# Optimization experiments

Measured on AMD Instinct MI355X. Metric: run time of the kernel, lower is better.

Reference implementation:

```python
import jax, jax.numpy as jnp
import numpy as np

EPS = 1e-06

def phi(x):
    # canonical linear-attention feature map: elu(x) + 1 (positive features)
    return jax.nn.elu(x) + 1.0

def setup_inputs() -> dict:
    key = jax.random.key(0)
    kq, kk, kv = jax.random.split(key, 3)
    B, H, S, D = 4, 16, 4096, 64
    query = jax.random.normal(kq, (B, H, S, D), dtype=jnp.float32)
    k = jax.random.normal(kk, (B, H, S, D), dtype=jnp.float32)
    value = jax.random.normal(kv, (B, H, S, D), dtype=jnp.float32)
    attention_mask = jnp.ones((B, S), dtype=jnp.float32)
    return {"query": query, "key": k, "value": value, "attention_mask": attention_mask}

def reference(query, key, value, attention_mask):
    B, H, S, D = query.shape
    q = query / jnp.sqrt(jnp.asarray(D, query.dtype))
    phi_q = phi(q)                                   # [b,h,n,d]
    phi_k = phi(key)                                 # [b,h,n,d]
    mask = attention_mask[:, None, :, None].astype(phi_k.dtype)  # [b,1,n,1]
    phi_k = phi_k * mask
    kv_term = jnp.einsum('bhnd,bhnv->bhdv', phi_k, value)        # [b,h,d,v]
    output = jnp.einsum('bhnd,bhdv->bhnv', phi_q, kv_term)       # [b,h,n,v]
    k_one = jnp.sum(phi_k, axis=2)                               # [b,h,d] == phi_k @ masked ones
    normalizer = jnp.einsum('bhnd,bhd->bhn', phi_q, k_one)[..., None]  # [b,h,n,1]
    return output / (normalizer + EPS)
```

## Files before the change

### kernel.cpp

```cpp
#include <hip/hip_runtime.h>

typedef unsigned short ushort_t;
typedef unsigned int uint32;
typedef __bf16 bf16x8 __attribute__((ext_vector_type(8)));
typedef float f32x4 __attribute__((ext_vector_type(4)));

#define NB 4
#define NH 16
#define NS 4096
#define ND 64
#define NBH 64
#define EPSF 1e-6f

#define CH1 16
#define ROWS1 (NS / CH1)
#define P2R 128
#define LDJ 70
#define LDJW 35

__device__ __forceinline__ float phi_f(float x) {
    return x > 0.0f ? x + 1.0f : __expf(x);
}
__device__ __forceinline__ ushort_t bf16_rn(float x) {
    uint32 u = __float_as_uint(x);
    uint32 r = (u + 0x7FFFu + ((u >> 16) & 1u)) >> 16;
    return (ushort_t)r;
}
__device__ __forceinline__ void split2(float x, ushort_t& h, ushort_t& l) {
    h = bf16_rn(x);
    float hf = __uint_as_float(((uint32)h) << 16);
    l = bf16_rn(x - hf);
}
union FragU { uint32 u[4]; bf16x8 v; };
__device__ __forceinline__ bf16x8 ld_frag(const ushort_t* arr, int widx) {
    const uint32* p = (const uint32*)arr;
    FragU f;
    f.u[0] = p[widx]; f.u[1] = p[widx + 1]; f.u[2] = p[widx + 2]; f.u[3] = p[widx + 3];
    return f.v;
}
__device__ __forceinline__ f32x4 mfma16(bf16x8 a, bf16x8 b, f32x4 c) {
    return __builtin_amdgcn_mfma_f32_16x16x32_bf16(a, b, c, 0, 0, 0);
}

template<bool PART>
__global__ __launch_bounds__(256)
void la_pass1(const float* __restrict__ Kin, const float* __restrict__ Vin,
              const float* __restrict__ Min, float* __restrict__ okv,
              float* __restrict__ ok1)
{
    const int t  = threadIdx.x;
    const int cx = blockIdx.x;
    const int bh = blockIdx.y;
    const int bb = bh >> 4;
    const float* Kb = Kin + (long long)bh * NS * ND;
    const float* Vb = Vin + (long long)bh * NS * ND;
    const float* Mb = Min + (long long)bb * NS;

    __shared__ __align__(16) ushort_t skh[64 * LDJ], skl[64 * LDJ];
    __shared__ __align__(16) ushort_t svh[64 * LDJ], svl[64 * LDJ];

    const int p  = t & 31;
    const int c0 = (t >> 5) * 8;
    const int wv = t >> 6;
    const int m  = t & 15;
    const int q  = (t & 63) >> 4;
    const int lane = t & 63;

    const f32x4 zf = {0.f, 0.f, 0.f, 0.f};
    f32x4 acc0 = zf, acc1 = zf, acc2 = zf, acc3 = zf;
    float k1loc[8] = {0.f,0.f,0.f,0.f,0.f,0.f,0.f,0.f};

    const int s0 = cx * ROWS1;

    for (int tile = 0; tile < ROWS1 / 64; ++tile) {
        const int rb = s0 + tile * 64;
        __syncthreads();
        {
            const int r0 = rb + 2 * p;
            const float4 ka = *(const float4*)(Kb + (long long)r0 * ND + c0);
            const float4 kb2 = *(const float4*)(Kb + (long long)r0 * ND + c0 + 4);
            const float4 kc = *(const float4*)(Kb + (long long)(r0 + 1) * ND + c0);
            const float4 kd = *(const float4*)(Kb + (long long)(r0 + 1) * ND + c0 + 4);
            const float4 va = *(const float4*)(Vb + (long long)r0 * ND + c0);
            const float4 vb2 = *(const float4*)(Vb + (long long)r0 * ND + c0 + 4);
            const float4 vc = *(const float4*)(Vb + (long long)(r0 + 1) * ND + c0);
            const float4 vd = *(const float4*)(Vb + (long long)(r0 + 1) * ND + c0 + 4);
            const float m0 = Mb[r0], m1 = Mb[r0 + 1];
            const float kr0[8] = {ka.x,ka.y,ka.z,ka.w,kb2.x,kb2.y,kb2.z,kb2.w};
            const float kr1[8] = {kc.x,kc.y,kc.z,kc.w,kd.x,kd.y,kd.z,kd.w};
            const float vr0[8] = {va.x,va.y,va.z,va.w,vb2.x,vb2.y,vb2.z,vb2.w};
            const float vr1[8] = {vc.x,vc.y,vc.z,vc.w,vd.x,vd.y,vd.z,vd.w};
            #pragma unroll
            for (int i = 0; i < 8; ++i) {
                const float x0 = phi_f(kr0[i]) * m0;
                const float x1 = phi_f(kr1[i]) * m1;
                k1loc[i] += x0 + x1;
                ushort_t h0, l0, h1, l1;
                split2(x0, h0, l0); split2(x1, h1, l1);
                const int widx = (c0 + i) * LDJW + p;
                ((uint32*)skh)[widx] = (uint32)h0 | ((uint32)h1 << 16);
                ((uint32*)skl)[widx] = (uint32)l0 | ((uint32)l1 << 16);
                split2(vr0[i], h0, l0); split2(vr1[i], h1, l1);
                ((uint32*)svh)[widx] = (uint32)h0 | ((uint32)h1 << 16);
                ((uint32*)svl)[widx] = (uint32)l0 | ((uint32)l1 << 16);
            }
        }
        __syncthreads();
        #pragma unroll
        for (int ks = 0; ks < 2; ++ks) {
            const int fo = ks * 16 + q * 4;
            const bf16x8 ah = ld_frag(skh, (16 * wv + m) * LDJW + fo);
            const bf16x8 al = ld_frag(skl, (16 * wv + m) * LDJW + fo);
            {
                const bf16x8 fbh = ld_frag(svh, (0 + m) * LDJW + fo);
                const bf16x8 fbl = ld_frag(svl, (0 + m) * LDJW + fo);
                acc0 = mfma16(al, fbh, acc0); acc0 = mfma16(ah, fbl, acc0); acc0 = mfma16(ah, fbh, acc0);
            }
            {
                const bf16x8 fbh = ld_frag(svh, (16 + m) * LDJW + fo);
                const bf16x8 fbl = ld_frag(svl, (16 + m) * LDJW + fo);
                acc1 = mfma16(al, fbh, acc1); acc1 = mfma16(ah, fbl, acc1); acc1 = mfma16(ah, fbh, acc1);
            }
            {
                const bf16x8 fbh = ld_frag(svh, (32 + m) * LDJW + fo);
                const bf16x8 fbl = ld_frag(svl, (32 + m) * LDJW + fo);
                acc2 = mfma16(al, fbh, acc2); acc2 = mfma16(ah, fbl, acc2); acc2 = mfma16(ah, fbh, acc2);
            }
            {
                const bf16x8 fbh = ld_frag(svh, (48 + m) * LDJW + fo);
                const bf16x8 fbl = ld_frag(svl, (48 + m) * LDJW + fo);
                acc3 = mfma16(al, fbh, acc3); acc3 = mfma16(ah, fbl, acc3); acc3 = mfma16(ah, fbh, acc3);
            }
        }
    }

    const int dbase = 16 * wv + q * 4;
    if (PART) {
        float* outp = okv + (long long)(bh * CH1 + cx) * (ND * ND);
        #pragma unroll
        for (int i = 0; i < 4; ++i) {
            outp[(dbase + i) * ND +  0 + m] = acc0[i];
            outp[(dbase + i) * ND + 16 + m] = acc1[i];
            outp[(dbase + i) * ND + 32 + m] = acc2[i];
            outp[(dbase + i) * ND + 48 + m] = acc3[i];
        }
    } else {
        float* outp = okv + (long long)bh * (ND * ND);
        #pragma unroll
        for (int i = 0; i < 4; ++i) {
            atomicAdd(&outp[(dbase + i) * ND +  0 + m], acc0[i]);
            atomicAdd(&outp[(dbase + i) * ND + 16 + m], acc1[i]);
            atomicAdd(&outp[(dbase + i) * ND + 32 + m], acc2[i]);
            atomicAdd(&outp[(dbase + i) * ND + 48 + m], acc3[i]);
        }
    }
    __syncthreads();
    float* red = (float*)skh;
    #pragma unroll
    for (int i = 0; i < 8; ++i) red[(c0 + i) * 33 + p] = k1loc[i];
    __syncthreads();
    if (t < 64) {
        float s = 0.f;
        #pragma unroll
        for (int pp = 0; pp < 32; ++pp) s += red[t * 33 + pp];
        if (PART) ok1[(bh * CH1 + cx) * ND + t] = s;
        else      atomicAdd(&ok1[bh * ND + t], s);
    }
}

__global__ __launch_bounds__(256)
void la_reduce(const float* __restrict__ pkv, const float* __restrict__ pk1,
               float* __restrict__ kv, float* __restrict__ k1)
{
    const int t = threadIdx.x;
    const int bh = blockIdx.x;
    const float4* src = (const float4*)(pkv + (long long)bh * CH1 * ND * ND);
    float4 a[4];
    #pragma unroll
    for (int i = 0; i < 4; ++i) { a[i].x = 0.f; a[i].y = 0.f; a[i].z = 0.f; a[i].w = 0.f; }
    for (int c = 0; c < CH1; ++c) {
        #pragma unroll
        for (int i = 0; i < 4; ++i) {
            const float4 v = src[c * 1024 + t + 256 * i];
            a[i].x += v.x; a[i].y += v.y; a[i].z += v.z; a[i].w += v.w;
        }
    }
    float4* dst = (float4*)(kv + (long long)bh * ND * ND);
    #pragma unroll
    for (int i = 0; i < 4; ++i) dst[t + 256 * i] = a[i];
    if (t < ND) {
        float s = 0.f;
        for (int c = 0; c < CH1; ++c) s += pk1[(bh * CH1 + c) * ND + t];
        k1[bh * ND + t] = s;
    }
}

__global__ __launch_bounds__(256)
void la_pass2(const float* __restrict__ Qin, const float* __restrict__ KVin,
              const float* __restrict__ K1in, float* __restrict__ Out)
{
    const int t  = threadIdx.x;
    const int bh = blockIdx.y;
    const int s0 = blockIdx.x * P2R;
    const long long base = (long long)bh * NS * ND;

    __shared__ __align__(16) ushort_t sAh[P2R * LDJ], sAl[P2R * LDJ];
    __shared__ __align__(16) ushort_t sBh[80 * LDJ],  sBl[80 * LDJ];

    {
        const float* KVb = KVin + (long long)bh * ND * ND;
        const int d  = t >> 4;
        const int v4 = (t & 15) * 4;
        #pragma unroll
        for (int it = 0; it < 4; ++it) {
            const int dd = d + 16 * it;
            const float4 kv = *(const float4*)(KVb + dd * ND + v4);
            const float vals[4] = {kv.x, kv.y, kv.z, kv.w};
            #pragma unroll
            for (int i = 0; i < 4; ++i) {
                ushort_t h, l; split2(vals[i], h, l);
                sBh[(v4 + i) * LDJ + dd] = h;
                sBl[(v4 + i) * LDJ + dd] = l;
            }
        }
        if (t < 64) {
            ushort_t h, l; split2(K1in[bh * ND + t], h, l);
            sBh[64 * LDJ + t] = h; sBl[64 * LDJ + t] = l;
        }
        for (int z = t; z < 15 * 64; z += 256) {
            const int n  = 65 + (z >> 6);
            const int dd = z & 63;
            sBh[n * LDJ + dd] = 0; sBl[n * LDJ + dd] = 0;
        }
    }
    {
        const int lr = t >> 4;
        const int lc = (t & 15) * 4;
        #pragma unroll
        for (int it = 0; it < 8; ++it) {
            const int r = lr + 16 * it;
            const float4 q4 = *(const float4*)(Qin + base + (long long)(s0 + r) * ND + lc);
            const float xs[4] = {q4.x, q4.y, q4.z, q4.w};
            ushort_t h[4], l[4];
            #pragma unroll
            for (int i = 0; i < 4; ++i) split2(phi_f(xs[i] * 0.125f), h[i], l[i]);
            const int w0 = (r * LDJ + lc) >> 1;
            ((uint32*)sAh)[w0]     = (uint32)h[0] | ((uint32)h[1] << 16);
            ((uint32*)sAh)[w0 + 1] = (uint32)h[2] | ((uint32)h[3] << 16);
            ((uint32*)sAl)[w0]     = (uint32)l[0] | ((uint32)l[1] << 16);
            ((uint32*)sAl)[w0 + 1] = (uint32)l[2] | ((uint32)l[3] << 16);
        }
    }
    __syncthreads();

    const int wv = t >> 6;
    const int m  = t & 15;
    const int q  = (t & 63) >> 4;
    const int lane = t & 63;

    const f32x4 zf = {0.f, 0.f, 0.f, 0.f};
    f32x4 acc[2][5];
    #pragma unroll
    for (int a = 0; a < 2; ++a)
        #pragma unroll
        for (int b = 0; b < 5; ++b) acc[a][b] = zf;

    #pragma unroll
    for (int ks = 0; ks < 2; ++ks) {
        const int fo = ks * 16 + q * 4;
        const bf16x8 a0h = ld_frag(sAh, (16 * (2 * wv + 0) + m) * LDJW + fo);
        const bf16x8 a0l = ld_frag(sAl, (16 * (2 * wv + 0) + m) * LDJW + fo);
        const bf16x8 a1h = ld_frag(sAh, (16 * (2 * wv + 1) + m) * LDJW + fo);
        const bf16x8 a1l = ld_frag(sAl, (16 * (2 * wv + 1) + m) * LDJW + fo);
        #pragma unroll
        for (int nt = 0; nt < 5; ++nt) {
            const bf16x8 fbh = ld_frag(sBh, (16 * nt + m) * LDJW + fo);
            const bf16x8 fbl = ld_frag(sBl, (16 * nt + m) * LDJW + fo);
            acc[0][nt] = mfma16(a0l, fbh, acc[0][nt]);
            acc[0][nt] = mfma16(a0h, fbl, acc[0][nt]);
            acc[0][nt] = mfma16(a0h, fbh, acc[0][nt]);
            acc[1][nt] = mfma16(a1l, fbh, acc[1][nt]);
            acc[1][nt] = mfma16(a1h, fbl, acc[1][nt]);
            acc[1][nt] = mfma16(a1h, fbh, acc[1][nt]);
        }
    }

    float* outb = Out + base;
    #pragma unroll
    for (int mtl = 0; mtl < 2; ++mtl) {
        const int rbase = s0 + 16 * (2 * wv + mtl) + q * 4;
        #pragma unroll
        for (int i = 0; i < 4; ++i) {
            const float nv = __shfl(acc[mtl][4][i], lane & 48, 64);
            const float rn = 1.0f / (nv + EPSF);
            const long long ro = (long long)(rbase + i) * ND;
            outb[ro +  0 + m] = acc[mtl][0][i] * rn;
            outb[ro + 16 + m] = acc[mtl][1][i] * rn;
            outb[ro + 32 + m] = acc[mtl][2][i] * rn;
            outb[ro + 48 + m] = acc[mtl][3][i] * rn;
        }
    }
}

extern "C" void kernel_launch(void* const* d_in, const int* in_sizes, int n_in,
                              void* d_out, int out_size, void* d_ws, size_t ws_size,
                              hipStream_t stream)
{
    const float* Q = (const float*)d_in[0];
    const float* K = (const float*)d_in[1];
    const float* V = (const float*)d_in[2];
    const float* M = (const float*)d_in[3];
    float* Out = (float*)d_out;

    const size_t partf = (size_t)NBH * CH1 * ND * ND;
    const size_t pk1f  = (size_t)NBH * CH1 * ND;
    const size_t kvf   = (size_t)NBH * ND * ND;
    const size_t k1f   = (size_t)NBH * ND;
    const size_t need  = (partf + pk1f + kvf + k1f) * sizeof(float);

    if (ws_size >= need) {
        float* PKV = (float*)d_ws;
        float* PK1 = PKV + partf;
        float* KVb = PK1 + pk1f;
        float* K1b = KVb + kvf;
        la_pass1<true><<<dim3(CH1, NBH), dim3(256), 0, stream>>>(K, V, M, PKV, PK1);
        la_reduce<<<dim3(NBH), dim3(256), 0, stream>>>(PKV, PK1, KVb, K1b);
        la_pass2<<<dim3(NS / P2R, NBH), dim3(256), 0, stream>>>(Q, KVb, K1b, Out);
    } else {
        float* KVb = (float*)d_ws;
        float* K1b = KVb + kvf;
        hipMemsetAsync(d_ws, 0, (kvf + k1f) * sizeof(float), stream);
        la_pass1<false><<<dim3(CH1, NBH), dim3(256), 0, stream>>>(K, V, M, KVb, K1b);
        la_pass2<<<dim3(NS / P2R, NBH), dim3(256), 0, stream>>>(Q, KVb, K1b, Out);
    }
}
```

Baseline: 243.1 us.

## Precompute split-bf16 KV once in reduce; pass2 loads fragments straight to registers

The reduce kernel now emits the KV matrix and k1 row already split into hi/lo bf16 and transposed, so pass2 no longer converts the KV state in every block. Pass2 also skips shared memory entirely: Q fragments are built in registers and B fragments are read directly from global memory. Pass1 software-prefetches the next K/V tile into registers while the current tile is processed, widens the LDS stride, uses vector fragment loads, and both kernels get occupancy hints. The cost is an extra convert kernel on the fallback path and uncoalesced-ish global fragment loads in pass2 that depend on cache hits.

```diff
diff --git a/kernel.cpp b/kernel.cpp
--- a/kernel.cpp
+++ b/kernel.cpp
@@ -15,8 +15,9 @@
 #define CH1 16
 #define ROWS1 (NS / CH1)
 #define P2R 128
-#define LDJ 70
-#define LDJW 35
+#define LDJ 72
+#define LDJW 36
+#define BTSZ (80 * 64)
 
 __device__ __forceinline__ float phi_f(float x) {
     return x > 0.0f ? x + 1.0f : __expf(x);
@@ -31,19 +32,16 @@
     float hf = __uint_as_float(((uint32)h) << 16);
     l = bf16_rn(x - hf);
 }
-union FragU { uint32 u[4]; bf16x8 v; };
+union FragP { ushort_t s[8]; bf16x8 v; };
 __device__ __forceinline__ bf16x8 ld_frag(const ushort_t* arr, int widx) {
-    const uint32* p = (const uint32*)arr;
-    FragU f;
-    f.u[0] = p[widx]; f.u[1] = p[widx + 1]; f.u[2] = p[widx + 2]; f.u[3] = p[widx + 3];
-    return f.v;
+    return *(const bf16x8*)((const uint32*)arr + widx);
 }
 __device__ __forceinline__ f32x4 mfma16(bf16x8 a, bf16x8 b, f32x4 c) {
     return __builtin_amdgcn_mfma_f32_16x16x32_bf16(a, b, c, 0, 0, 0);
 }
 
 template<bool PART>
-__global__ __launch_bounds__(256)
+__global__ __launch_bounds__(256, 4)
 void la_pass1(const float* __restrict__ Kin, const float* __restrict__ Vin,
               const float* __restrict__ Min, float* __restrict__ okv,
               float* __restrict__ ok1)
@@ -64,7 +62,6 @@
     const int wv = t >> 6;
     const int m  = t & 15;
     const int q  = (t & 63) >> 4;
-    const int lane = t & 63;
 
     const f32x4 zf = {0.f, 0.f, 0.f, 0.f};
     f32x4 acc0 = zf, acc1 = zf, acc2 = zf, acc3 = zf;
@@ -72,39 +69,49 @@
 
     const int s0 = cx * ROWS1;
 
+    float4 ka, kb2, kc, kd, va, vb2, vc, vd;
+    float m0, m1;
+#define LOADT(tt) { \
+        const int r0_ = s0 + (tt) * 64 + 2 * p; \
+        const float* kp_ = Kb + (long long)r0_ * ND + c0; \
+        const float* vp_ = Vb + (long long)r0_ * ND + c0; \
+        ka  = *(const float4*)kp_;        kb2 = *(const float4*)(kp_ + 4); \
+        kc  = *(const float4*)(kp_ + ND); kd  = *(const float4*)(kp_ + ND + 4); \
+        va  = *(const float4*)vp_;        vb2 = *(const float4*)(vp_ + 4); \
+        vc  = *(const float4*)(vp_ + ND); vd  = *(const float4*)(vp_ + ND + 4); \
+        m0 = Mb[r0_]; m1 = Mb[r0_ + 1]; }
+
+    LOADT(0);
+
     for (int tile = 0; tile < ROWS1 / 64; ++tile) {
-        const int rb = s0 + tile * 64;
+        const float kr0[8] = {ka.x,ka.y,ka.z,ka.w,kb2.x,kb2.y,kb2.z,kb2.w};
+        const float kr1[8] = {kc.x,kc.y,kc.z,kc.w,kd.x,kd.y,kd.z,kd.w};
+        const float vr0[8] = {va.x,va.y,va.z,va.w,vb2.x,vb2.y,vb2.z,vb2.w};
+        const float vr1[8] = {vc.x,vc.y,vc.z,vc.w,vd.x,vd.y,vd.z,vd.w};
+        uint32 wkh[8], wkl[8], wvh[8], wvl[8];
+        #pragma unroll
+        for (int i = 0; i < 8; ++i) {
+            const float x0 = phi_f(kr0[i]) * m0;
+            const float x1 = phi_f(kr1[i]) * m1;
+            k1loc[i] += x0 + x1;
+            ushort_t h0, l0, h1, l1;
+            split2(x0, h0, l0); split2(x1, h1, l1);
+            wkh[i] = (uint32)h0 | ((uint32)h1 << 16);
+            wkl[i] = (uint32)l0 | ((uint32)l1 << 16);
+            split2(vr0[i], h0, l0); split2(vr1[i], h1, l1);
+            wvh[i] = (uint32)h0 | ((uint32)h1 << 16);
+            wvl[i] = (uint32)l0 | ((uint32)l1 << 16);
+        }
         __syncthreads();
-        {
-            const int r0 = rb + 2 * p;
-            const float4 ka = *(const float4*)(Kb + (long long)r0 * ND + c0);
-            const float4 kb2 = *(const float4*)(Kb + (long long)r0 * ND + c0 + 4);
-            const float4 kc = *(const float4*)(Kb + (long long)(r0 + 1) * ND + c0);
-            const float4 kd = *(const float4*)(Kb + (long long)(r0 + 1) * ND + c0 + 4);
-            const float4 va = *(const float4*)(Vb + (long long)r0 * ND + c0);
-            const float4 vb2 = *(const float4*)(Vb + (long long)r0 * ND + c0 + 4);
-            const float4 vc = *(const float4*)(Vb + (long long)(r0 + 1) * ND + c0);
-            const float4 vd = *(const float4*)(Vb + (long long)(r0 + 1) * ND + c0 + 4);
-            const float m0 = Mb[r0], m1 = Mb[r0 + 1];
-            const float kr0[8] = {ka.x,ka.y,ka.z,ka.w,kb2.x,kb2.y,kb2.z,kb2.w};
-            const float kr1[8] = {kc.x,kc.y,kc.z,kc.w,kd.x,kd.y,kd.z,kd.w};
-            const float vr0[8] = {va.x,va.y,va.z,va.w,vb2.x,vb2.y,vb2.z,vb2.w};
-            const float vr1[8] = {vc.x,vc.y,vc.z,vc.w,vd.x,vd.y,vd.z,vd.w};
-            #pragma unroll
-            for (int i = 0; i < 8; ++i) {
-                const float x0 = phi_f(kr0[i]) * m0;
-                const float x1 = phi_f(kr1[i]) * m1;
-                k1loc[i] += x0 + x1;
-                ushort_t h0, l0, h1, l1;
-                split2(x0, h0, l0); split2(x1, h1, l1);
-                const int widx = (c0 + i) * LDJW + p;
-                ((uint32*)skh)[widx] = (uint32)h0 | ((uint32)h1 << 16);
-                ((uint32*)skl)[widx] = (uint32)l0 | ((uint32)l1 << 16);
-                split2(vr0[i], h0, l0); split2(vr1[i], h1, l1);
-                ((uint32*)svh)[widx] = (uint32)h0 | ((uint32)h1 << 16);
-                ((uint32*)svl)[widx] = (uint32)l0 | ((uint32)l1 << 16);
-            }
-        }
+        #pragma unroll
+        for (int i = 0; i < 8; ++i) {
+            const int widx = (c0 + i) * LDJW + p;
+            ((uint32*)skh)[widx] = wkh[i];
+            ((uint32*)skl)[widx] = wkl[i];
+            ((uint32*)svh)[widx] = wvh[i];
+            ((uint32*)svl)[widx] = wvl[i];
+        }
+        if (tile + 1 < ROWS1 / 64) LOADT(tile + 1);
         __syncthreads();
         #pragma unroll
         for (int ks = 0; ks < 2; ++ks) {
@@ -133,6 +140,7 @@
             }
         }
     }
+#undef LOADT
 
     const int dbase = 16 * wv + q * 4;
     if (PART) {
@@ -170,7 +178,7 @@
 
 __global__ __launch_bounds__(256)
 void la_reduce(const float* __restrict__ pkv, const float* __restrict__ pk1,
-               float* __restrict__ kv, float* __restrict__ k1)
+               ushort_t* __restrict__ BTh, ushort_t* __restrict__ BTl)
 {
     const int t = threadIdx.x;
     const int bh = blockIdx.x;
@@ -185,78 +193,82 @@
             a[i].x += v.x; a[i].y += v.y; a[i].z += v.z; a[i].w += v.w;
         }
     }
-    float4* dst = (float4*)(kv + (long long)bh * ND * ND);
-    #pragma unroll
-    for (int i = 0; i < 4; ++i) dst[t + 256 * i] = a[i];
+    ushort_t* oh = BTh + (long long)bh * BTSZ;
+    ushort_t* ol = BTl + (long long)bh * BTSZ;
+    #pragma unroll
+    for (int i = 0; i < 4; ++i) {
+        const int e4 = t + 256 * i;
+        const int d  = e4 >> 4;
+        const int v0 = (e4 & 15) * 4;
+        const float vals[4] = {a[i].x, a[i].y, a[i].z, a[i].w};
+        #pragma unroll
+        for (int j = 0; j < 4; ++j) {
+            ushort_t h, l; split2(vals[j], h, l);
+            oh[(v0 + j) * ND + d] = h;
+            ol[(v0 + j) * ND + d] = l;
+        }
+    }
     if (t < ND) {
         float s = 0.f;
         for (int c = 0; c < CH1; ++c) s += pk1[(bh * CH1 + c) * ND + t];
-        k1[bh * ND + t] = s;
-    }
+        ushort_t h, l; split2(s, h, l);
+        oh[64 * ND + t] = h; ol[64 * ND + t] = l;
+    }
+    for (int z = t; z < 15 * 64; z += 256) { oh[65 * ND + z] = 0; ol[65 * ND + z] = 0; }
 }
 
 __global__ __launch_bounds__(256)
-void la_pass2(const float* __restrict__ Qin, const float* __restrict__ KVin,
-              const float* __restrict__ K1in, float* __restrict__ Out)
+void la_convert(const float* __restrict__ kv, const float* __restrict__ k1,
+                ushort_t* __restrict__ BTh, ushort_t* __restrict__ BTl)
+{
+    const int t = threadIdx.x;
+    const int bh = blockIdx.x;
+    const float* kvb = kv + (long long)bh * ND * ND;
+    ushort_t* oh = BTh + (long long)bh * BTSZ;
+    ushort_t* ol = BTl + (long long)bh * BTSZ;
+    for (int e = t; e < ND * ND; e += 256) {
+        const int d = e >> 6, v = e & 63;
+        ushort_t h, l; split2(kvb[e], h, l);
+        oh[v * ND + d] = h; ol[v * ND + d] = l;
+    }
+    if (t < ND) { ushort_t h, l; split2(k1[bh * ND + t], h, l); oh[64 * ND + t] = h; ol[64 * ND + t] = l; }
+    for (int z = t; z < 15 * 64; z += 256) { oh[65 * ND + z] = 0; ol[65 * ND + z] = 0; }
+}
+
+__global__ __launch_bounds__(256, 4)
+void la_pass2(const float* __restrict__ Qin, const ushort_t* __restrict__ BTh,
+              const ushort_t* __restrict__ BTl, float* __restrict__ Out)
 {
     const int t  = threadIdx.x;
     const int bh = blockIdx.y;
     const int s0 = blockIdx.x * P2R;
     const long long base = (long long)bh * NS * ND;
-
-    __shared__ __align__(16) ushort_t sAh[P2R * LDJ], sAl[P2R * LDJ];
-    __shared__ __align__(16) ushort_t sBh[80 * LDJ],  sBl[80 * LDJ];
-
-    {
-        const float* KVb = KVin + (long long)bh * ND * ND;
-        const int d  = t >> 4;
-        const int v4 = (t & 15) * 4;
-        #pragma unroll
-        for (int it = 0; it < 4; ++it) {
-            const int dd = d + 16 * it;
-            const float4 kv = *(const float4*)(KVb + dd * ND + v4);
-            const float vals[4] = {kv.x, kv.y, kv.z, kv.w};
-            #pragma unroll
-            for (int i = 0; i < 4; ++i) {
-                ushort_t h, l; split2(vals[i], h, l);
-                sBh[(v4 + i) * LDJ + dd] = h;
-                sBl[(v4 + i) * LDJ + dd] = l;
-            }
-        }
-        if (t < 64) {
-            ushort_t h, l; split2(K1in[bh * ND + t], h, l);
-            sBh[64 * LDJ + t] = h; sBl[64 * LDJ + t] = l;
-        }
-        for (int z = t; z < 15 * 64; z += 256) {
-            const int n  = 65 + (z >> 6);
-            const int dd = z & 63;
-            sBh[n * LDJ + dd] = 0; sBl[n * LDJ + dd] = 0;
-        }
-    }
-    {
-        const int lr = t >> 4;
-        const int lc = (t & 15) * 4;
-        #pragma unroll
-        for (int it = 0; it < 8; ++it) {
-            const int r = lr + 16 * it;
-            const float4 q4 = *(const float4*)(Qin + base + (long long)(s0 + r) * ND + lc);
-            const float xs[4] = {q4.x, q4.y, q4.z, q4.w};
-            ushort_t h[4], l[4];
-            #pragma unroll
-            for (int i = 0; i < 4; ++i) split2(phi_f(xs[i] * 0.125f), h[i], l[i]);
-            const int w0 = (r * LDJ + lc) >> 1;
-            ((uint32*)sAh)[w0]     = (uint32)h[0] | ((uint32)h[1] << 16);
-            ((uint32*)sAh)[w0 + 1] = (uint32)h[2] | ((uint32)h[3] << 16);
-            ((uint32*)sAl)[w0]     = (uint32)l[0] | ((uint32)l[1] << 16);
-            ((uint32*)sAl)[w0 + 1] = (uint32)l[2] | ((uint32)l[3] << 16);
-        }
-    }
-    __syncthreads();
-
     const int wv = t >> 6;
     const int m  = t & 15;
     const int q  = (t & 63) >> 4;
     const int lane = t & 63;
+    const ushort_t* Bh = BTh + (long long)bh * BTSZ;
+    const ushort_t* Bl = BTl + (long long)bh * BTSZ;
+
+    bf16x8 aH[2][2], aL[2][2];
+    #pragma unroll
+    for (int mtl = 0; mtl < 2; ++mtl) {
+        const int row = s0 + 32 * wv + 16 * mtl + m;
+        const float* qp = Qin + base + (long long)row * ND;
+        #pragma unroll
+        for (int ks = 0; ks < 2; ++ks) {
+            const float4 x0 = *(const float4*)(qp + ks * 32 + q * 8);
+            const float4 x1 = *(const float4*)(qp + ks * 32 + q * 8 + 4);
+            const float xs[8] = {x0.x,x0.y,x0.z,x0.w,x1.x,x1.y,x1.z,x1.w};
+            FragP fh, fl;
+            #pragma unroll
+            for (int i = 0; i < 8; ++i) {
+                ushort_t h, l; split2(phi_f(xs[i] * 0.125f), h, l);
+                fh.s[i] = h; fl.s[i] = l;
+            }
+            aH[mtl][ks] = fh.v; aL[mtl][ks] = fl.v;
+        }
+    }
 
     const f32x4 zf = {0.f, 0.f, 0.f, 0.f};
     f32x4 acc[2][5];
@@ -267,28 +279,24 @@
 
     #pragma unroll
     for (int ks = 0; ks < 2; ++ks) {
-        const int fo = ks * 16 + q * 4;
-        const bf16x8 a0h = ld_frag(sAh, (16 * (2 * wv + 0) + m) * LDJW + fo);
-        const bf16x8 a0l = ld_frag(sAl, (16 * (2 * wv + 0) + m) * LDJW + fo);
-        const bf16x8 a1h = ld_frag(sAh, (16 * (2 * wv + 1) + m) * LDJW + fo);
-        const bf16x8 a1l = ld_frag(sAl, (16 * (2 * wv + 1) + m) * LDJW + fo);
         #pragma unroll
         for (int nt = 0; nt < 5; ++nt) {
-            const bf16x8 fbh = ld_frag(sBh, (16 * nt + m) * LDJW + fo);
-            const bf16x8 fbl = ld_frag(sBl, (16 * nt + m) * LDJW + fo);
-            acc[0][nt] = mfma16(a0l, fbh, acc[0][nt]);
-            acc[0][nt] = mfma16(a0h, fbl, acc[0][nt]);
-            acc[0][nt] = mfma16(a0h, fbh, acc[0][nt]);
-            acc[1][nt] = mfma16(a1l, fbh, acc[1][nt]);
-            acc[1][nt] = mfma16(a1h, fbl, acc[1][nt]);
-            acc[1][nt] = mfma16(a1h, fbh, acc[1][nt]);
+            const int bo = (16 * nt + m) * ND + ks * 32 + q * 8;
+            const bf16x8 fbh = *(const bf16x8*)(Bh + bo);
+            const bf16x8 fbl = *(const bf16x8*)(Bl + bo);
+            acc[0][nt] = mfma16(aL[0][ks], fbh, acc[0][nt]);
+            acc[0][nt] = mfma16(aH[0][ks], fbl, acc[0][nt]);
+            acc[0][nt] = mfma16(aH[0][ks], fbh, acc[0][nt]);
+            acc[1][nt] = mfma16(aL[1][ks], fbh, acc[1][nt]);
+            acc[1][nt] = mfma16(aH[1][ks], fbl, acc[1][nt]);
+            acc[1][nt] = mfma16(aH[1][ks], fbh, acc[1][nt]);
         }
     }
 
     float* outb = Out + base;
     #pragma unroll
     for (int mtl = 0; mtl < 2; ++mtl) {
-        const int rbase = s0 + 16 * (2 * wv + mtl) + q * 4;
+        const int rbase = s0 + 32 * wv + 16 * mtl + q * 4;
         #pragma unroll
         for (int i = 0; i < 4; ++i) {
             const float nv = __shfl(acc[mtl][4][i], lane & 48, 64);
@@ -316,21 +324,25 @@
     const size_t pk1f  = (size_t)NBH * CH1 * ND;
     const size_t kvf   = (size_t)NBH * ND * ND;
     const size_t k1f   = (size_t)NBH * ND;
-    const size_t need  = (partf + pk1f + kvf + k1f) * sizeof(float);
+    const size_t btu   = (size_t)NBH * BTSZ;
+    const size_t need  = (partf + pk1f) * sizeof(float) + 2 * btu * sizeof(ushort_t);
 
     if (ws_size >= need) {
         float* PKV = (float*)d_ws;
         float* PK1 = PKV + partf;
-        float* KVb = PK1 + pk1f;
-        float* K1b = KVb + kvf;
+        ushort_t* BThp = (ushort_t*)(PK1 + pk1f);
+        ushort_t* BTlp = BThp + btu;
         la_pass1<true><<<dim3(CH1, NBH), dim3(256), 0, stream>>>(K, V, M, PKV, PK1);
-        la_reduce<<<dim3(NBH), dim3(256), 0, stream>>>(PKV, PK1, KVb, K1b);
-        la_pass2<<<dim3(NS / P2R, NBH), dim3(256), 0, stream>>>(Q, KVb, K1b, Out);
+        la_reduce<<<dim3(NBH), dim3(256), 0, stream>>>(PKV, PK1, BThp, BTlp);
+        la_pass2<<<dim3(NS / P2R, NBH), dim3(256), 0, stream>>>(Q, BThp, BTlp, Out);
     } else {
         float* KVb = (float*)d_ws;
         float* K1b = KVb + kvf;
+        ushort_t* BThp = (ushort_t*)(K1b + k1f);
+        ushort_t* BTlp = BThp + btu;
         hipMemsetAsync(d_ws, 0, (kvf + k1f) * sizeof(float), stream);
         la_pass1<false><<<dim3(CH1, NBH), dim3(256), 0, stream>>>(K, V, M, KVb, K1b);
-        la_pass2<<<dim3(NS / P2R, NBH), dim3(256), 0, stream>>>(Q, KVb, K1b, Out);
-    }
-}
+        la_convert<<<dim3(NBH), dim3(256), 0, stream>>>(KVb, K1b, BThp, BTlp);
+        la_pass2<<<dim3(NS / P2R, NBH), dim3(256), 0, stream>>>(Q, BThp, BTlp, Out);
+    }
+}
```

Measured after the change: 249.1 us. +2.5%, slower.
